# Kernel optimization log

Measured on AMD Instinct MI355X. Metric: run time of the kernel, lower is better.

## Reference

```python
import itertools
import jax, jax.numpy as jnp
import numpy as np

GRID = (41, 1600, 1408)   # KITTI voxel grid (z, y, x)
N_VOX = 80000
C_IN, C_OUT = 32, 64
NEG_SLOPE = 0.01          # nn.LeakyReLU default
BN_EPS = 1e-5

# ---------- numpy rulebook construction (spconv indice pairs) ----------

def _lin(c, grid):
    return (c[:, 0] * grid[1] + c[:, 1]) * grid[2] + c[:, 2]

def _lookup(lin_sorted, q, valid):
    pos = np.searchsorted(lin_sorted, q)
    pos = np.clip(pos, 0, len(lin_sorted) - 1)
    found = valid & (lin_sorted[pos] == q)
    return np.where(found, pos, len(lin_sorted)).astype(np.int32)  # sentinel = N

def _offsets(kshape, d):
    rs = [([-d, 0, d] if s == 3 else [0]) for s in kshape]
    return list(itertools.product(*rs))

def _subm_map(coords, lin_sorted, grid, kshape, d):
    offs = _offsets(kshape, d)
    g = np.asarray(grid)
    nbr = np.empty((len(offs), len(coords)), np.int32)
    for k, off in enumerate(offs):
        q = coords + np.asarray(off)
        valid = ((q >= 0) & (q < g)).all(1)
        nbr[k] = _lookup(lin_sorted, _lin(q, grid), valid)
    return nbr

def _build_maps(seed=0):
    rng = np.random.default_rng(seed)
    tot = GRID[0] * GRID[1] * GRID[2]
    lin0 = np.sort(rng.choice(tot, size=N_VOX, replace=False))
    c0 = np.stack(np.unravel_index(lin0, GRID), axis=1).astype(np.int64)
    nbr331_d1 = _subm_map(c0, lin0, GRID, (3, 3, 1), 1)
    nbr313_d1 = _subm_map(c0, lin0, GRID, (3, 1, 3), 1)
    # SparseConv3d k=3 s=2 p=1: output active sites = union over inputs/offsets
    og = tuple((g + 2 - 3) // 2 + 1 for g in GRID)
    offs27 = np.asarray(list(itertools.product(range(3), repeat=3)))
    cand = c0[None, :, :] + 1 - offs27[:, None, :]
    ok = (cand % 2 == 0).all(-1)
    p = cand // 2
    ok &= ((p >= 0) & (p < np.asarray(og))).all(-1)
    plin = (p[..., 0] * og[1] + p[..., 1]) * og[2] + p[..., 2]
    lin1 = np.unique(plin[ok])
    c1 = np.stack(np.unravel_index(lin1, og), axis=1).astype(np.int64)
    M = len(c1)
    pool_nbr = np.empty((27, M), np.int32)
    gg = np.asarray(GRID)
    for k in range(27):
        q = c1 * 2 - 1 + offs27[k]
        valid = ((q >= 0) & (q < gg)).all(1)
        pool_nbr[k] = _lookup(lin0, _lin(q, GRID), valid)
    nbr331_d2 = _subm_map(c1, lin1, og, (3, 3, 1), 2)
    nbr313_d2 = _subm_map(c1, lin1, og, (3, 1, 3), 2)
    nbr331_d3 = _subm_map(c1, lin1, og, (3, 3, 1), 3)
    nbr313_d3 = _subm_map(c1, lin1, og, (3, 1, 3), 3)
    maps = dict(nbr331_d1=jnp.asarray(nbr331_d1), nbr313_d1=jnp.asarray(nbr313_d1),
                pool_nbr=jnp.asarray(pool_nbr), nbr331_d2=jnp.asarray(nbr331_d2),
                nbr313_d2=jnp.asarray(nbr313_d2), nbr331_d3=jnp.asarray(nbr331_d3),
                nbr313_d3=jnp.asarray(nbr313_d3))
    return maps, M

# ---------- jax forward ----------

def _subm(f, nbr, W):
    # gather-GEMM-scatter sparse conv: out[n] = sum_k f[nbr[k,n]] @ W[k]
    padf = jnp.concatenate([f, jnp.zeros((1, f.shape[1]), f.dtype)], 0)  # zero row for missing nbr
    out = jnp.zeros((nbr.shape[1], W.shape[2]), f.dtype)
    for k in range(nbr.shape[0]):  # fixed small kernel-volume loop (9 or 27)
        out = out + padf[nbr[k]] @ W[k]
    return out

def _bn_act(x):
    # BatchNorm1d (training stats, gamma=1, beta=0 per weight_initialization) + LeakyReLU
    m = jnp.mean(x, 0)
    v = jnp.var(x, 0)
    return jax.nn.leaky_relu((x - m) * jax.lax.rsqrt(v + BN_EPS), NEG_SLOPE)

def _res(f, nA, nB, w1, w12, w2, w22):
    # nA: (3,3,1) map (conv3x1), nB: (3,1,3) map (conv1x3)
    s = _bn_act(_subm(f, nA, w1))
    s = _bn_act(_subm(s, nB, w12))
    r = _bn_act(_subm(f, nB, w2))
    r = _bn_act(_subm(r, nA, w22))
    return r + s

def setup_inputs() -> dict:
    maps, M = _build_maps()
    ks = jax.random.split(jax.random.key(0), 16)
    def w(k, shape):
        fan = shape[-2] * (shape[0] if len(shape) == 3 else 1)
        return jax.random.normal(k, shape, jnp.float32) / np.sqrt(fan)
    inp = dict(
        feats=jax.random.normal(ks[0], (N_VOX, C_IN), jnp.float32),
        b1_w1=w(ks[1], (9, C_IN, C_OUT)), b1_w1_2=w(ks[2], (9, C_OUT, C_OUT)),
        b1_w2=w(ks[3], (9, C_IN, C_OUT)), b1_w2_2=w(ks[4], (9, C_OUT, C_OUT)),
        pool_w=w(ks[5], (27, C_OUT, C_OUT)),
        b2_w1=w(ks[6], (9, C_OUT, C_OUT)), b2_w1_2=w(ks[7], (9, C_OUT, C_OUT)),
        b2_w2=w(ks[8], (9, C_OUT, C_OUT)), b2_w2_2=w(ks[9], (9, C_OUT, C_OUT)),
        b3_w1=w(ks[10], (9, C_OUT, C_OUT)), b3_w1_2=w(ks[11], (9, C_OUT, C_OUT)),
        b3_w2=w(ks[12], (9, C_OUT, C_OUT)), b3_w2_2=w(ks[13], (9, C_OUT, C_OUT)),
        down_w=w(ks[14], (3 * C_OUT, C_OUT)),
    )
    inp.update(maps)
    return inp

def reference(feats, b1_w1, b1_w1_2, b1_w2, b1_w2_2, pool_w,
              b2_w1, b2_w1_2, b2_w2, b2_w2_2,
              b3_w1, b3_w1_2, b3_w2, b3_w2_2, down_w,
              nbr331_d1, nbr313_d1, pool_nbr,
              nbr331_d2, nbr313_d2, nbr331_d3, nbr313_d3):
    x1 = _res(feats, nbr331_d1, nbr313_d1, b1_w1, b1_w1_2, b1_w2, b1_w2_2)
    x1 = _subm(x1, pool_nbr, pool_w)                     # strided SparseConv3d pool -> [M, C]
    x2 = _res(x1, nbr331_d2, nbr313_d2, b2_w1, b2_w1_2, b2_w2, b2_w2_2)  # dilation 2
    x3 = _res(x2, nbr331_d3, nbr313_d3, b3_w1, b3_w1_2, b3_w2, b3_w2_2)  # dilation 3
    return jnp.concatenate([x1, x2, x3], -1) @ down_w     # 1x1 subm conv fuse
```

## Files before the change

### kernel.cpp

```cpp
#include <hip/hip_runtime.h>
#include <hip/hip_bf16.h>

#define NEG 0.01f
#define BN_EPS 1e-5f

typedef __hip_bfloat16 bf16;
typedef __attribute__((ext_vector_type(8))) short short8;
typedef __attribute__((ext_vector_type(16))) float f32x16;

__device__ __forceinline__ float b2f(short s) {
    unsigned u = ((unsigned)(unsigned short)s) << 16;
    float f;
    __builtin_memcpy(&f, &u, 4);
    return f;
}
__device__ __forceinline__ short f2b(float f) {
    union { bf16 b; short s; } t;
    t.b = __float2bfloat16(f);
    return t.s;
}

__global__ void finalize2_k(const float* __restrict__ sA, const float* __restrict__ sB,
                            float* __restrict__ fA, float* __restrict__ fB,
                            float inv_n) {
    const float* s = blockIdx.x == 0 ? sA : sB;
    float* f = blockIdx.x == 0 ? fA : fB;
    int c = threadIdx.x;
    float sm = 0.f, sq = 0.f;
    #pragma unroll
    for (int k = 0; k < 32; ++k) {
        sm += s[k * 256 + c];
        sq += s[k * 256 + 64 + c];
    }
    float m = sm * inv_n;
    float v = sq * inv_n - m * m;
    f[c] = m;
    f[64 + c] = rsqrtf(v + BN_EPS);
}


__global__ __launch_bounds__(256) void bnact2_k(
    bf16* __restrict__ xa, const float* __restrict__ fa,
    bf16* __restrict__ xb, const float* __restrict__ fb, int nvec) {
    int i = blockIdx.x * blockDim.x + threadIdx.x;
    if (i >= 2 * nvec) return;
    bf16* x; const float* f; int j;
    if (i < nvec) { x = xa; f = fa; j = i; }
    else          { x = xb; f = fb; j = i - nvec; }
    const int c0 = (j & 7) << 3;
    short8 v = *reinterpret_cast<const short8*>(x + ((size_t)j << 3));
    short8 o;
    #pragma unroll
    for (int e = 0; e < 8; ++e) {
        float t = (b2f(v[e]) - f[c0 + e]) * f[64 + c0 + e];
        t = t > 0.f ? t : NEG * t;
        o[e] = f2b(t);
    }
    *reinterpret_cast<short8*>(x + ((size_t)j << 3)) = o;
}

__global__ __launch_bounds__(256) void bnadd_k(
    const bf16* __restrict__ a, const float* __restrict__ fa,
    const bf16* __restrict__ b, const float* __restrict__ fb,
    bf16* __restrict__ out, int nvec) {
    int i = blockIdx.x * blockDim.x + threadIdx.x;
    if (i >= nvec) return;
    const int c0 = (i & 7) << 3;
    short8 va = *reinterpret_cast<const short8*>(a + ((size_t)i << 3));
    short8 vb = *reinterpret_cast<const short8*>(b + ((size_t)i << 3));
    short8 o;
    #pragma unroll
    for (int e = 0; e < 8; ++e) {
        float ta = (b2f(va[e]) - fa[c0 + e]) * fa[64 + c0 + e];
        ta = ta > 0.f ? ta : NEG * ta;
        float tb = (b2f(vb[e]) - fb[c0 + e]) * fb[64 + c0 + e];
        tb = tb > 0.f ? tb : NEG * tb;
        o[e] = f2b(ta + tb);
    }
    *reinterpret_cast<short8*>(out + ((size_t)i << 3)) = o;
}

__global__ void cvt_f32_bf16_k(const float* __restrict__ x, bf16* __restrict__ y, int n) {
    int i = blockIdx.x * blockDim.x + threadIdx.x;
    if (i < n) y[i] = __float2bfloat16(x[i]);
}

struct PackEnt { const float* src; bf16* dst; int kt; int ns; };
struct PackArgs { PackEnt e[16]; };

__global__ void pack_w_k(PackArgs pa) {
    PackEnt E = pa.e[blockIdx.y];
    int cin = E.ns * 16;
    int total = E.kt * E.ns * 1024;
    for (int i = blockIdx.x * blockDim.x + threadIdx.x; i < total;
         i += gridDim.x * blockDim.x) {
        int j = i & 7, lane = (i >> 3) & 63, c = (i >> 9) & 1;
        int rem = i >> 10;
        int s = rem % E.ns, k = rem / E.ns;
        int krow = s * 16 + ((lane >> 5) << 3) + j;
        int col = c * 32 + (lane & 31);
        E.dst[i] = __float2bfloat16(E.src[((size_t)k * cin + krow) * 64 + col]);
    }
}

struct Job {
    const bf16* fin; const int* nbr; const bf16* Wp; bf16* out; float* stat;
    int n_out, n_in;
};
struct Jobs { Job j[2]; int t_split, t_total; };
struct Jobs4 { Job j[2]; int b_split; };

template <int NS, int K>
__global__ __launch_bounds__(512, 4) void mconv4(Jobs4 jb) {
    __shared__ short8 WL[K * NS * 128];
    const int CIN = NS * 16;
    const int tid = threadIdx.x;
    const int lane = tid & 63;
    const int col = lane & 31;
    const int q = lane >> 5;
    const int widl = tid >> 6;
    const int nwl = blockDim.x >> 6;

    const int nb = gridDim.x;
    const int qq = nb >> 3, rr = nb & 7;
    const int xcd = blockIdx.x & 7, bi = blockIdx.x >> 3;
    const int sb = (xcd < rr) ? xcd * (qq + 1) + bi
                              : rr * (qq + 1) + (xcd - rr) * qq + bi;

    const int jsel = (sb >= jb.b_split) ? 1 : 0;
    const Job J = jb.j[jsel];
    const int lb = jsel ? sb - jb.b_split : sb;
    const int nbj = jsel ? nb - jb.b_split : jb.b_split;
    const int ntiles = (J.n_out + 31) >> 5;

    {
        const short8* wsrc = (const short8*)J.Wp;
        for (int i = tid; i < K * NS * 128; i += blockDim.x) WL[i] = wsrc[i];
    }
    __syncthreads();

    const int wid = lb * nwl + widl;
    const int nw = nbj * nwl;

    for (int tile = wid; tile < ntiles; tile += nw) {
        const int rbase = tile << 5;
        const int r = rbase + col;
        const bool rowok = r < J.n_out;

        f32x16 acc0, acc1;
        #pragma unroll
        for (int i = 0; i < 16; ++i) { acc0[i] = 0.f; acc1[i] = 0.f; }

        int idx[K];
        #pragma unroll
        for (int t = 0; t < K; ++t)
            idx[t] = rowok ? J.nbr[(size_t)t * J.n_out + r] : J.n_in;

        auto loadA = [&](int id, short8 (&dst)[NS]) {
            const bool v = id < J.n_in;
            const bf16* src = J.fin + (size_t)id * CIN + q * 8;
            #pragma unroll
            for (int s = 0; s < NS; ++s) {
                short8 z = {0, 0, 0, 0, 0, 0, 0, 0};
                dst[s] = z;
                if (v) dst[s] = *(const short8*)(src + s * 16);
            }
        };
        auto dotap = [&](int k, int id, short8 (&a)[NS]) {
            if (__ballot(id < J.n_in) == 0ull) return;
            #pragma unroll
            for (int s = 0; s < NS; ++s) {
                short8 b0 = WL[((k * NS + s) * 2 + 0) * 64 + lane];
                short8 b1 = WL[((k * NS + s) * 2 + 1) * 64 + lane];
                acc0 = __builtin_amdgcn_mfma_f32_32x32x16_bf16(a[s], b0, acc0, 0, 0, 0);
                acc1 = __builtin_amdgcn_mfma_f32_32x32x16_bf16(a[s], b1, acc1, 0, 0, 0);
            }
        };

        short8 A0[NS], A1[NS];
        loadA(idx[0], A0);
        #pragma unroll 1
        for (int t = 0; t + 2 <= K; t += 2) {
            loadA(idx[t + 1], A1);
            dotap(t, idx[t], A0);
            if (t + 2 < K) loadA(idx[t + 2], A0);
            dotap(t + 1, idx[t + 1], A1);
        }
        dotap(K - 1, idx[K - 1], A0);

        float s0 = 0.f, q0 = 0.f, s1 = 0.f, q1 = 0.f;
        #pragma unroll
        for (int i = 0; i < 16; ++i) {
            int row = (i & 3) + 8 * (i >> 2) + 4 * q;
            int gr = rbase + row;
            if (gr < J.n_out) {
                float v0 = acc0[i], v1 = acc1[i];
                J.out[(size_t)gr * 64 + col] = __float2bfloat16(v0);
                J.out[(size_t)gr * 64 + 32 + col] = __float2bfloat16(v1);
                s0 += v0; q0 += v0 * v0;
                s1 += v1; q1 += v1 * v1;
            }
        }
        if (J.stat != nullptr) {
            s0 += __shfl_xor(s0, 32); q0 += __shfl_xor(q0, 32);
            s1 += __shfl_xor(s1, 32); q1 += __shfl_xor(q1, 32);
            float* st = J.stat + (((sb << 3) + widl) & 31) * 256;
            if (q == 0) {
                atomicAdd(&st[col], s0);
                atomicAdd(&st[64 + col], q0);
            } else {
                atomicAdd(&st[32 + col], s1);
                atomicAdd(&st[96 + col], q1);
            }
        }
    }
}

template <int NS, int K>
__global__ __launch_bounds__(256, 6) void mconv3(Jobs jb) {
    const int CIN = NS * 16;
    const int lane = threadIdx.x & 63;
    const int col = lane & 31;
    const int q = lane >> 5;

    const int nb = gridDim.x;
    const int qq = nb >> 3, rr = nb & 7;
    const int xcd = blockIdx.x & 7, bi = blockIdx.x >> 3;
    const int sb = (xcd < rr) ? xcd * (qq + 1) + bi
                              : rr * (qq + 1) + (xcd - rr) * qq + bi;

    const int wid = sb * (blockDim.x >> 6) + (threadIdx.x >> 6);
    const int nw = gridDim.x * (blockDim.x >> 6);

    for (int tg = wid; tg < jb.t_total; tg += nw) {
        const int jsel = (tg >= jb.t_split) ? 1 : 0;
        const Job J = jb.j[jsel];
        const int tile = tg - (jsel ? jb.t_split : 0);
        const int rbase = tile << 5;
        const int r = rbase + col;
        const bool rowok = r < J.n_out;

        f32x16 acc0, acc1;
        #pragma unroll
        for (int i = 0; i < 16; ++i) { acc0[i] = 0.f; acc1[i] = 0.f; }

        #pragma unroll
        for (int g = 0; g < K / 9; ++g) {
            int idx[9];
            #pragma unroll
            for (int t = 0; t < 9; ++t)
                idx[t] = rowok ? J.nbr[(size_t)(g * 9 + t) * J.n_out + r] : J.n_in;

            #pragma unroll 1
            for (int t = 0; t < 9; ++t) {
                const bool v = idx[t] < J.n_in;
                if (__ballot(v) == 0ull) continue;
                const int k = g * 9 + t;
                const bf16* src = J.fin + (size_t)idx[t] * CIN + q * 8;
                const short8* wp = (const short8*)J.Wp + (size_t)k * (NS * 128) + lane;
                #pragma unroll
                for (int s = 0; s < NS; ++s) {
                    short8 a;
                    if (v) a = *(const short8*)(src + s * 16);
                    else { short8 z = {0,0,0,0,0,0,0,0}; a = z; }
                    short8 b0 = wp[(s * 2 + 0) * 64];
                    short8 b1 = wp[(s * 2 + 1) * 64];
                    acc0 = __builtin_amdgcn_mfma_f32_32x32x16_bf16(a, b0, acc0, 0, 0, 0);
                    acc1 = __builtin_amdgcn_mfma_f32_32x32x16_bf16(a, b1, acc1, 0, 0, 0);
                }
            }
        }

        #pragma unroll
        for (int i = 0; i < 16; ++i) {
            int row = (i & 3) + 8 * (i >> 2) + 4 * q;
            int gr = rbase + row;
            if (gr < J.n_out) {
                J.out[(size_t)gr * 64 + col] = __float2bfloat16(acc0[i]);
                J.out[(size_t)gr * 64 + 32 + col] = __float2bfloat16(acc1[i]);
            }
        }
    }
}

__global__ __launch_bounds__(256, 6) void down_k(
    const bf16* __restrict__ x1, const bf16* __restrict__ x2,
    const bf16* __restrict__ x3, const bf16* __restrict__ W1,
    const bf16* __restrict__ W2, const bf16* __restrict__ W3,
    float* __restrict__ out, int m) {
    const int lane = threadIdx.x & 63;
    const int col = lane & 31;
    const int q = lane >> 5;
    const int wid = blockIdx.x * (blockDim.x >> 6) + (threadIdx.x >> 6);
    const int nw = gridDim.x * (blockDim.x >> 6);
    const int ntiles = (m + 31) >> 5;

    for (int tile = wid; tile < ntiles; tile += nw) {
        const int rbase = tile << 5;
        const int r = rbase + col;
        const bool rowok = r < m;

        f32x16 acc0, acc1;
        #pragma unroll
        for (int i = 0; i < 16; ++i) { acc0[i] = 0.f; acc1[i] = 0.f; }

        const bf16* xs[3] = {x1, x2, x3};
        const bf16* ws[3] = {W1, W2, W3};
        #pragma unroll 1
        for (int t = 0; t < 3; ++t) {
            const bf16* src = xs[t] + (size_t)r * 64 + q * 8;
            const short8* wp = (const short8*)ws[t] + lane;
            #pragma unroll
            for (int s = 0; s < 4; ++s) {
                short8 a;
                if (rowok) a = *(const short8*)(src + s * 16);
                else { short8 z = {0,0,0,0,0,0,0,0}; a = z; }
                short8 b0 = wp[(s * 2 + 0) * 64];
                short8 b1 = wp[(s * 2 + 1) * 64];
                acc0 = __builtin_amdgcn_mfma_f32_32x32x16_bf16(a, b0, acc0, 0, 0, 0);
                acc1 = __builtin_amdgcn_mfma_f32_32x32x16_bf16(a, b1, acc1, 0, 0, 0);
            }
        }
        #pragma unroll
        for (int i = 0; i < 16; ++i) {
            int row = (i & 3) + 8 * (i >> 2) + 4 * q;
            int gr = rbase + row;
            if (gr < m) {
                out[(size_t)gr * 64 + col] = acc0[i];
                out[(size_t)gr * 64 + 32 + col] = acc1[i];
            }
        }
    }
}


extern "C" void kernel_launch(void* const* d_in, const int* in_sizes, int n_in_,
                              void* d_out, int out_size, void* d_ws,
                              size_t ws_size, hipStream_t stream) {
    const float* feats = (const float*)d_in[0];
    const float* Wsrc[16] = {
        (const float*)d_in[1], (const float*)d_in[2],
        (const float*)d_in[3], (const float*)d_in[4],
        (const float*)d_in[5],
        (const float*)d_in[6], (const float*)d_in[7],
        (const float*)d_in[8], (const float*)d_in[9],
        (const float*)d_in[10], (const float*)d_in[11],
        (const float*)d_in[12], (const float*)d_in[13],
        (const float*)d_in[14],
        (const float*)d_in[14] + 64 * 64,
        (const float*)d_in[14] + 128 * 64,
    };
    const int kts[16] = {9,9,9,9, 27, 9,9,9,9, 9,9,9,9, 1,1,1};
    const int nss[16] = {2,4,2,4,  4, 4,4,4,4, 4,4,4,4, 4,4,4};

    const int* nA1 = (const int*)d_in[15];
    const int* nB1 = (const int*)d_in[16];
    const int* pnbr = (const int*)d_in[17];
    const int* nA2 = (const int*)d_in[18];
    const int* nB2 = (const int*)d_in[19];
    const int* nA3 = (const int*)d_in[20];
    const int* nB3 = (const int*)d_in[21];

    const int N = in_sizes[0] / 32;
    const int M = in_sizes[17] / 27;
    const size_t MX = (size_t)(N > M ? N : M);

    bf16* A = (bf16*)d_ws;
    bf16* B = A + MX * 64;
    bf16* C = B + MX * 64;
    bf16* D = C + MX * 64;
    bf16* E = D + MX * 64;
    bf16* FB = E + MX * 64;
    bf16* WP = FB + (size_t)N * 32;
    bf16* G = (bf16*)d_out;
    bf16* Wp[16];
    {
        size_t off = 0;
        for (int i = 0; i < 16; ++i) {
            Wp[i] = WP + off;
            off += (size_t)kts[i] * nss[i] * 1024;
        }
    }
    size_t wp_total = 0;
    for (int i = 0; i < 16; ++i) wp_total += (size_t)kts[i] * nss[i] * 1024;
    float* ST = (float*)(WP + wp_total + (wp_total & 1));
    float* FS = ST + (size_t)12 * 32 * 256;
    float* out = (float*)d_out;
    auto S = [&](int i) { return ST + (size_t)i * 32 * 256; };
    auto F = [&](int i) { return FS + (size_t)i * 128; };

    hipMemsetAsync(ST, 0, (size_t)12 * 32 * 256 * sizeof(float), stream);
    {
        PackArgs pa;
        for (int i = 0; i < 16; ++i) pa.e[i] = {Wsrc[i], Wp[i], kts[i], nss[i]};
        pack_w_k<<<dim3(64, 16), 256, 0, stream>>>(pa);
    }
    cvt_f32_bf16_k<<<(N * 32 + 255) / 256, 256, 0, stream>>>(feats, FB, N * 32);

    const float invN = 1.f / (float)N, invM = 1.f / (float)M;
    const int nvN = N * 8, nvM = M * 8;

    auto mkjob = [](const bf16* fin, const int* nbr, const bf16* w, bf16* o,
                    float* st, int no, int ni) {
        Job j; j.fin = fin; j.nbr = nbr; j.Wp = w; j.out = o; j.stat = st;
        j.n_out = no; j.n_in = ni; return j;
    };
    auto pair4 = [&](void (*kp)(Jobs4), Job a, Job b) {
        Jobs4 jb; jb.j[0] = a; jb.j[1] = b;
        const int nb = 512;
        long ta = (a.n_out + 31) >> 5, tb = (b.n_out + 31) >> 5;
        int bs = (int)((ta * nb + (ta + tb) / 2) / (ta + tb));
        if (bs < 1) bs = 1;
        if (bs > nb - 1) bs = nb - 1;
        jb.b_split = bs;
        hipLaunchKernelGGL(kp, dim3(nb), dim3(512), 0, stream, jb);
    };
    auto single = [&](void (*kp)(Jobs), Job a) {
        Jobs jb; jb.j[0] = a; jb.j[1] = a;
        int ta = (a.n_out + 31) >> 5;
        jb.t_split = ta; jb.t_total = ta;
        int blocks = (ta + 3) >> 2;
        hipLaunchKernelGGL(kp, dim3(blocks), dim3(256), 0, stream, jb);
    };

    pair4(mconv4<2, 9>,
          mkjob(FB, nA1, Wp[0], A, S(0), N, N),
          mkjob(FB, nB1, Wp[2], B, S(2), N, N));
    finalize2_k<<<2, 64, 0, stream>>>(S(0), S(2), F(0), F(2), invN);
    bnact2_k<<<(2 * nvN + 255) / 256, 256, 0, stream>>>(A, F(0), B, F(2), nvN);
    pair4(mconv4<4, 9>,
          mkjob(A, nB1, Wp[1], C, S(1), N, N),
          mkjob(B, nA1, Wp[3], E, S(3), N, N));
    finalize2_k<<<2, 64, 0, stream>>>(S(1), S(3), F(1), F(3), invN);
    bnadd_k<<<(nvN + 255) / 256, 256, 0, stream>>>(C, F(1), E, F(3), B, nvN);

    single(mconv3<4, 27>, mkjob(B, pnbr, Wp[4], D, nullptr, M, N));

    pair4(mconv4<4, 9>,
          mkjob(D, nA2, Wp[5], A, S(4), M, M),
          mkjob(D, nB2, Wp[7], B, S(6), M, M));
    finalize2_k<<<2, 64, 0, stream>>>(S(4), S(6), F(4), F(6), invM);
    bnact2_k<<<(2 * nvM + 255) / 256, 256, 0, stream>>>(A, F(4), B, F(6), nvM);
    pair4(mconv4<4, 9>,
          mkjob(A, nB2, Wp[6], C, S(5), M, M),
          mkjob(B, nA2, Wp[8], E, S(7), M, M));
    finalize2_k<<<2, 64, 0, stream>>>(S(5), S(7), F(5), F(7), invM);
    bnadd_k<<<(nvM + 255) / 256, 256, 0, stream>>>(C, F(5), E, F(7), E, nvM);

    pair4(mconv4<4, 9>,
          mkjob(E, nA3, Wp[9], A, S(8), M, M),
          mkjob(E, nB3, Wp[11], B, S(10), M, M));
    finalize2_k<<<2, 64, 0, stream>>>(S(8), S(10), F(8), F(10), invM);
    bnact2_k<<<(2 * nvM + 255) / 256, 256, 0, stream>>>(A, F(8), B, F(10), nvM);
    pair4(mconv4<4, 9>,
          mkjob(A, nB3, Wp[10], C, S(9), M, M),
          mkjob(B, nA3, Wp[12], G, S(11), M, M));
    finalize2_k<<<2, 64, 0, stream>>>(S(9), S(11), F(9), F(11), invM);
    bnadd_k<<<(nvM + 255) / 256, 256, 0, stream>>>(C, F(9), G, F(11), B, nvM);

    {
        int blocks = (((M + 31) >> 5) + 3) >> 2;
        down_k<<<blocks, 256, 0, stream>>>(D, E, B, Wp[13], Wp[14], Wp[15], out, M);
    }
}
```

Measured before the change: 604.9 us.

## Rewrite strided pool conv to stage weights in LDS and double-buffer gathers

Replaces the generic mconv3 pool convolution with a dedicated mpool_k kernel. It uses 512-thread blocks that copy each 9-tap group of weights into shared memory and reuse it across 8 warps, instead of each warp reading weights from global memory. Feature gathers are double-buffered so the next tap's rows load while MFMAs run on the current one, and the grid is a fixed 512 blocks looping over tile batches. The cost is extra __syncthreads per group and more register pressure from the two A buffers.

```diff
diff --git a/kernel.cpp b/kernel.cpp
--- a/kernel.cpp
+++ b/kernel.cpp
@@ -107,7 +107,6 @@
     const bf16* fin; const int* nbr; const bf16* Wp; bf16* out; float* stat;
     int n_out, n_in;
 };
-struct Jobs { Job j[2]; int t_split, t_total; };
 struct Jobs4 { Job j[2]; int b_split; };
 
 template <int NS, int K>
@@ -216,12 +215,18 @@
     }
 }
 
-template <int NS, int K>
-__global__ __launch_bounds__(256, 6) void mconv3(Jobs jb) {
+template <int NS>
+__global__ __launch_bounds__(512, 4) void mpool_k(
+    const bf16* __restrict__ fin, const int* __restrict__ nbr,
+    const bf16* __restrict__ Wp, bf16* __restrict__ out,
+    int n_out, int n_in) {
+    __shared__ short8 WL[9 * NS * 128];
     const int CIN = NS * 16;
-    const int lane = threadIdx.x & 63;
+    const int tid = threadIdx.x;
+    const int lane = tid & 63;
     const int col = lane & 31;
     const int q = lane >> 5;
+    const int widl = tid >> 6;
 
     const int nb = gridDim.x;
     const int qq = nb >> 3, rr = nb & 7;
@@ -229,55 +234,75 @@
     const int sb = (xcd < rr) ? xcd * (qq + 1) + bi
                               : rr * (qq + 1) + (xcd - rr) * qq + bi;
 
-    const int wid = sb * (blockDim.x >> 6) + (threadIdx.x >> 6);
-    const int nw = gridDim.x * (blockDim.x >> 6);
-
-    for (int tg = wid; tg < jb.t_total; tg += nw) {
-        const int jsel = (tg >= jb.t_split) ? 1 : 0;
-        const Job J = jb.j[jsel];
-        const int tile = tg - (jsel ? jb.t_split : 0);
+    const int ntiles = (n_out + 31) >> 5;
+    const int nbatch = (ntiles + 7) >> 3;
+
+    for (int batch = sb; batch < nbatch; batch += nb) {
+        const int tile = (batch << 3) + widl;
         const int rbase = tile << 5;
         const int r = rbase + col;
-        const bool rowok = r < J.n_out;
+        const bool rowok = (tile < ntiles) && (r < n_out);
 
         f32x16 acc0, acc1;
         #pragma unroll
         for (int i = 0; i < 16; ++i) { acc0[i] = 0.f; acc1[i] = 0.f; }
 
-        #pragma unroll
-        for (int g = 0; g < K / 9; ++g) {
+        auto loadA = [&](int id, short8 (&dst)[NS]) {
+            const bool v = id < n_in;
+            const bf16* src = fin + (size_t)id * CIN + q * 8;
+            #pragma unroll
+            for (int s = 0; s < NS; ++s) {
+                short8 z = {0, 0, 0, 0, 0, 0, 0, 0};
+                dst[s] = z;
+                if (v) dst[s] = *(const short8*)(src + s * 16);
+            }
+        };
+        auto dotap = [&](int k, int id, short8 (&a)[NS]) {
+            if (__ballot(id < n_in) == 0ull) return;
+            #pragma unroll
+            for (int s = 0; s < NS; ++s) {
+                short8 b0 = WL[((k * NS + s) * 2 + 0) * 64 + lane];
+                short8 b1 = WL[((k * NS + s) * 2 + 1) * 64 + lane];
+                acc0 = __builtin_amdgcn_mfma_f32_32x32x16_bf16(a[s], b0, acc0, 0, 0, 0);
+                acc1 = __builtin_amdgcn_mfma_f32_32x32x16_bf16(a[s], b1, acc1, 0, 0, 0);
+            }
+        };
+
+        #pragma unroll 1
+        for (int g = 0; g < 3; ++g) {
+            __syncthreads();
+            {
+                const short8* wsrc = (const short8*)Wp + (size_t)g * (9 * NS * 128);
+                #pragma unroll
+                for (int i = 0; i < (9 * NS * 128) / 512; ++i)
+                    WL[i * 512 + tid] = wsrc[i * 512 + tid];
+            }
+            __syncthreads();
+
             int idx[9];
             #pragma unroll
             for (int t = 0; t < 9; ++t)
-                idx[t] = rowok ? J.nbr[(size_t)(g * 9 + t) * J.n_out + r] : J.n_in;
-
+                idx[t] = rowok ? nbr[(size_t)(g * 9 + t) * n_out + r] : n_in;
+
+            short8 A0[NS], A1[NS];
+            loadA(idx[0], A0);
             #pragma unroll 1
-            for (int t = 0; t < 9; ++t) {
-                const bool v = idx[t] < J.n_in;
-                if (__ballot(v) == 0ull) continue;
-                const int k = g * 9 + t;
-                const bf16* src = J.fin + (size_t)idx[t] * CIN + q * 8;
-                const short8* wp = (const short8*)J.Wp + (size_t)k * (NS * 128) + lane;
-                #pragma unroll
-                for (int s = 0; s < NS; ++s) {
-                    short8 a;
-                    if (v) a = *(const short8*)(src + s * 16);
-                    else { short8 z = {0,0,0,0,0,0,0,0}; a = z; }
-                    short8 b0 = wp[(s * 2 + 0) * 64];
-                    short8 b1 = wp[(s * 2 + 1) * 64];
-                    acc0 = __builtin_amdgcn_mfma_f32_32x32x16_bf16(a, b0, acc0, 0, 0, 0);
-                    acc1 = __builtin_amdgcn_mfma_f32_32x32x16_bf16(a, b1, acc1, 0, 0, 0);
-                }
-            }
+            for (int t = 0; t + 2 <= 9; t += 2) {
+                loadA(idx[t + 1], A1);
+                dotap(t, idx[t], A0);
+                if (t + 2 < 9) loadA(idx[t + 2], A0);
+                dotap(t + 1, idx[t + 1], A1);
+            }
+            dotap(8, idx[8], A0);
         }
 
         #pragma unroll
         for (int i = 0; i < 16; ++i) {
             int row = (i & 3) + 8 * (i >> 2) + 4 * q;
             int gr = rbase + row;
-            if (gr < J.n_out) {
-                J.out[(size_t)gr * 64 + col] = __float2bfloat16(acc0[i]);
-                J.out[(size_t)gr * 64 + 32 + col] = __float2bfloat16(acc1[i]);
+            if (tile < ntiles && gr < n_out) {
+                out[(size_t)gr * 64 + col] = __float2bfloat16(acc0[i]);
+                out[(size_t)gr * 64 + 32 + col] = __float2bfloat16(acc1[i]);
             }
         }
     }
@@ -415,13 +440,6 @@
         jb.b_split = bs;
         hipLaunchKernelGGL(kp, dim3(nb), dim3(512), 0, stream, jb);
     };
-    auto single = [&](void (*kp)(Jobs), Job a) {
-        Jobs jb; jb.j[0] = a; jb.j[1] = a;
-        int ta = (a.n_out + 31) >> 5;
-        jb.t_split = ta; jb.t_total = ta;
-        int blocks = (ta + 3) >> 2;
-        hipLaunchKernelGGL(kp, dim3(blocks), dim3(256), 0, stream, jb);
-    };
 
     pair4(mconv4<2, 9>,
           mkjob(FB, nA1, Wp[0], A, S(0), N, N),
@@ -434,7 +452,7 @@
     finalize2_k<<<2, 64, 0, stream>>>(S(1), S(3), F(1), F(3), invN);
     bnadd_k<<<(nvN + 255) / 256, 256, 0, stream>>>(C, F(1), E, F(3), B, nvN);
 
-    single(mconv3<4, 27>, mkjob(B, pnbr, Wp[4], D, nullptr, M, N));
+    mpool_k<4><<<512, 512, 0, stream>>>(B, pnbr, Wp[4], D, M, N);
 
     pair4(mconv4<4, 9>,
           mkjob(D, nA2, Wp[5], A, S(4), M, M),
```

Result: no change. 602.6 us (-0.4%).
